# Optimization experiments

Hardware: AMD Instinct MI355X
Metric: run time of the kernel (lower is better)

The kernel has to match this reference:

```python
import jax, jax.numpy as jnp
import numpy as np

B, N, T, C, H = 4, 1024, 12, 256, 8
DK = C // H
SCALE = 1.0 / np.sqrt(DK)


def setup_inputs() -> dict:
    key = jax.random.key(0)
    ks = jax.random.split(key, 16)
    names = ["flow_q", "flow_k", "flow_v", "speed_q", "speed_k", "speed_v"]
    inp = {n: jax.random.normal(ks[i], (B, N, T, C), dtype=jnp.float32) for i, n in enumerate(names)}
    w_scale = 1.0 / np.sqrt(C)  # ~kaiming-uniform-ish magnitude for Linear(C, C)
    wnames = ["w_fq", "w_fk", "w_fv", "w_sq", "w_sk", "w_sv", "w_out"]
    for j, n in enumerate(wnames):
        inp[n] = jax.random.normal(ks[6 + j], (C, C), dtype=jnp.float32) * w_scale
    inp["b_out"] = jnp.zeros((C,), dtype=jnp.float32)
    xav = np.sqrt(2.0 / (T + 1))  # xavier_normal for (T,1) params
    inp["kj"] = jax.random.normal(ks[13], (T, 1), dtype=jnp.float32) * xav
    inp["vf_fs"] = jax.random.normal(ks[14], (T, 1), dtype=jnp.float32) * xav
    return inp


def _heads(x, w):
    # x: [B,N,T,C], w: [C,C] (torch Linear: y = x @ w.T) -> [B,H,N,T,DK]
    y = jnp.einsum('bntc,oc->bnto', x, w)
    return y.reshape(B, N, T, H, DK).transpose(0, 3, 1, 2, 4)


def reference(flow_q, flow_k, flow_v, speed_q, speed_k, speed_v,
              w_fq, w_fk, w_fv, w_sq, w_sk, w_sv, w_out, b_out, kj, vf_fs):
    Qf = _heads(flow_q, w_fq)
    Kf = _heads(flow_k, w_fk)
    Vf = _heads(flow_v, w_fv)
    Qs = _heads(speed_q, w_sq)
    Ks = _heads(speed_k, w_sk)
    Vs = _heads(speed_v, w_sv)

    # FlowSpeed physics transform: Kj * (v - v^2 / (Vf + 1e-5)); (T,1) broadcasts over (T, DK)
    qf_from_speed = kj * (Qs - jnp.square(Qs) / (vf_fs + 1e-5))

    def att(a, b):  # scores over temporal axis: [B,H,N,T,T] -> softmax
        return jax.nn.softmax(jnp.einsum('bhntd,bhnsd->bhnts', a, b) * SCALE, axis=-1)

    def ctx(z, v):
        return jnp.einsum('bhnts,bhnsd->bhntd', z, v)

    z_ff = att(Qf, Kf)
    z_fs = att(Kf, qf_from_speed)
    z_sf = att(Ks, Qf)
    z_ss = att(Qs, Ks)

    def out_proj(c):  # [B,H,N,T,DK] -> [B,N,T,C] -> fc_out (shared weights)
        c = c.transpose(0, 2, 3, 1, 4).reshape(B, N, T, C)
        return jnp.einsum('bntc,oc->bnto', c, w_out) + b_out

    return (out_proj(ctx(z_ff, Vf)),
            out_proj(ctx(z_fs, Vf)),
            out_proj(ctx(z_sf, Vs)),
            out_proj(ctx(z_ss, Vs)))
```

## Files before the change

kernel.cpp:

```cpp
#include <hip/hip_runtime.h>

#define Bn 4
#define Nn 1024
#define Tn 12
#define Cn 256
#define Hn 8
#define DKn 32
#define Mrows 49152
#define NEl 12582912LL
#define SCALE_ 0.17677669529663687f

typedef __attribute__((ext_vector_type(4))) float f32x4;
typedef __attribute__((ext_vector_type(8))) short s16x8;
typedef __attribute__((ext_vector_type(4))) short s16x4;

__device__ __forceinline__ ushort f2bfu(float x) {
    unsigned u = __builtin_bit_cast(unsigned, x);
    u += 0x7fffu + ((u >> 16) & 1u);
    return (ushort)(u >> 16);
}
__device__ __forceinline__ float bfu2f(ushort h) {
    return __builtin_bit_cast(float, ((unsigned)h) << 16);
}

struct WPtrs { const float* src[7]; };

__global__ __launch_bounds__(256)
void wconv_k(WPtrs w, ushort* __restrict__ Wh, ushort* __restrict__ Wl) {
    int idx = blockIdx.x * 256 + threadIdx.x;
    int which = idx >> 16, pos = idx & 65535;
    float x = w.src[which][pos];
    ushort h = f2bfu(x);
    Wh[idx] = h;
    Wl[idx] = f2bfu(x - bfu2f(h));
}

struct GPtrs {
    const void*   A[4];
    const ushort* Wh[4];
    const ushort* Wl[4];
    void*         Y[4];
};

template<bool SPLIT, bool IN_BF16, bool OUT_BF16, bool BIAS>
__global__ __launch_bounds__(256)
void gemm_k(GPtrs p, const float* __restrict__ bias) {
    const int bt   = blockIdx.y;
    const int bm   = blockIdx.x * 64;
    const int tid  = threadIdx.x;
    const int lane = tid & 63;
    const int wave = tid >> 6;

    __shared__ short As[64 * 40];
    __shared__ short Bs[256 * 40];
    __shared__ short Al[SPLIT ? 64 * 40 : 8];
    __shared__ short Bl[SPLIT ? 256 * 40 : 8];

    f32x4 acc[4][4];
#pragma unroll
    for (int i = 0; i < 4; i++)
#pragma unroll
        for (int j = 0; j < 4; j++)
            acc[i][j] = (f32x4){0.f, 0.f, 0.f, 0.f};

    const int r  = tid >> 2;
    const int cq = (tid & 3) * 8;

    for (int k0 = 0; k0 < 256; k0 += 32) {
        if constexpr (IN_BF16) {
            const ushort* A = (const ushort*)p.A[bt];
            s16x8 v = *(const s16x8*)(A + (size_t)(bm + r) * 256 + k0 + cq);
            *(s16x8*)&As[r * 40 + cq] = v;
        } else {
            const float* A = (const float*)p.A[bt];
            const float* g = A + (size_t)(bm + r) * 256 + k0 + cq;
            f32x4 v0 = *(const f32x4*)g;
            f32x4 v1 = *(const f32x4*)(g + 4);
            s16x8 hi, lo;
#pragma unroll
            for (int j = 0; j < 8; j++) {
                float x = (j < 4) ? v0[j] : v1[j - 4];
                ushort hb = f2bfu(x);
                hi[j] = (short)hb;
                if constexpr (SPLIT) lo[j] = (short)f2bfu(x - bfu2f(hb));
            }
            *(s16x8*)&As[r * 40 + cq] = hi;
            if constexpr (SPLIT) *(s16x8*)&Al[r * 40 + cq] = lo;
        }
#pragma unroll
        for (int pw = 0; pw < 4; pw++) {
            int orow = pw * 64 + r;
            *(s16x8*)&Bs[orow * 40 + cq] =
                *(const s16x8*)(p.Wh[bt] + (size_t)orow * 256 + k0 + cq);
            if constexpr (SPLIT)
                *(s16x8*)&Bl[orow * 40 + cq] =
                    *(const s16x8*)(p.Wl[bt] + (size_t)orow * 256 + k0 + cq);
        }
        __syncthreads();
        s16x8 a[4], al[4];
#pragma unroll
        for (int mi = 0; mi < 4; mi++) {
            int off = (mi * 16 + (lane & 15)) * 40 + (lane >> 4) * 8;
            a[mi] = *(const s16x8*)&As[off];
            if constexpr (SPLIT) al[mi] = *(const s16x8*)&Al[off];
        }
#pragma unroll
        for (int ni = 0; ni < 4; ni++) {
            int off = (wave * 64 + ni * 16 + (lane & 15)) * 40 + (lane >> 4) * 8;
            s16x8 b = *(const s16x8*)&Bs[off];
            s16x8 bl;
            if constexpr (SPLIT) bl = *(const s16x8*)&Bl[off];
#pragma unroll
            for (int mi = 0; mi < 4; mi++) {
                acc[mi][ni] = __builtin_amdgcn_mfma_f32_16x16x32_bf16(a[mi], b, acc[mi][ni], 0, 0, 0);
                if constexpr (SPLIT) {
                    acc[mi][ni] = __builtin_amdgcn_mfma_f32_16x16x32_bf16(al[mi], b,  acc[mi][ni], 0, 0, 0);
                    acc[mi][ni] = __builtin_amdgcn_mfma_f32_16x16x32_bf16(a[mi],  bl, acc[mi][ni], 0, 0, 0);
                }
            }
        }
        __syncthreads();
    }
#pragma unroll
    for (int mi = 0; mi < 4; mi++) {
#pragma unroll
        for (int ni = 0; ni < 4; ni++) {
            int col  = wave * 64 + ni * 16 + (lane & 15);
            int row0 = bm + mi * 16 + (lane >> 4) * 4;
            float bv = BIAS ? bias[col] : 0.f;
#pragma unroll
            for (int rg = 0; rg < 4; rg++) {
                float v = acc[mi][ni][rg] + bv;
                size_t idx = (size_t)(row0 + rg) * 256 + col;
                if constexpr (OUT_BF16) ((ushort*)p.Y[bt])[idx] = f2bfu(v);
                else                    ((float*)p.Y[bt])[idx]  = v;
            }
        }
    }
}


#define VSTR 268

__device__ __forceinline__ s16x8 zero8() { s16x8 z = {0,0,0,0,0,0,0,0}; return z; }

__device__ __forceinline__ void split8(f32x4 a, f32x4 b, s16x8& hi, s16x8& lo) {
#pragma unroll
    for (int j = 0; j < 8; j++) {
        float x = (j < 4) ? a[j] : b[j - 4];
        ushort h = f2bfu(x);
        hi[j] = (short)h;
        lo[j] = (short)f2bfu(x - bfu2f(h));
    }
}

__device__ __forceinline__ void softmax_swapped(f32x4 acc, int g, s16x8& ph, s16x8& pl) {
    float x0 = acc[0] * SCALE_, x1 = acc[1] * SCALE_;
    float x2 = acc[2] * SCALE_, x3 = acc[3] * SCALE_;
    float m = fmaxf(fmaxf(x0, x1), fmaxf(x2, x3));
    m = fmaxf(m, __shfl_xor(m, 16));
    m = fmaxf(m, __shfl_xor(m, 32));
    float e0 = expf(x0 - m), e1 = expf(x1 - m), e2 = expf(x2 - m), e3 = expf(x3 - m);
    if (g == 3) { e0 = 0.f; e1 = 0.f; e2 = 0.f; e3 = 0.f; }
    float s = e0 + e1 + e2 + e3;
    s += __shfl_xor(s, 16);
    s += __shfl_xor(s, 32);
    float inv = 1.f / s;
    float p0 = e0 * inv, p1 = e1 * inv, p2 = e2 * inv, p3 = e3 * inv;
    float q0 = __shfl_down(p0, 16), q1 = __shfl_down(p1, 16);
    float q2 = __shfl_down(p2, 16), q3 = __shfl_down(p3, 16);
    float w[8];
    if (g == 0) { w[0]=p0; w[1]=p1; w[2]=p2; w[3]=p3; w[4]=q0; w[5]=q1; w[6]=q2; w[7]=q3; }
    else if (g == 1) { w[0]=q0; w[1]=q1; w[2]=q2; w[3]=q3; w[4]=0.f; w[5]=0.f; w[6]=0.f; w[7]=0.f; }
    else { w[0]=0.f; w[1]=0.f; w[2]=0.f; w[3]=0.f; w[4]=0.f; w[5]=0.f; w[6]=0.f; w[7]=0.f; }
#pragma unroll
    for (int j = 0; j < 8; j++) {
        ushort h = f2bfu(w[j]);
        ph[j] = (short)h;
        pl[j] = (short)f2bfu(w[j] - bfu2f(h));
    }
}

__device__ __forceinline__ s16x8 load_vfrag(const ushort* sV, int col, int g) {
    s16x8 v = zero8();
    if (g < 2) {
#pragma unroll
        for (int j = 0; j < 8; j++) {
            int s = 8 * g + j;
            if (s < 12) v[j] = (short)sV[s * VSTR + col];
        }
    }
    return v;
}

__device__ __forceinline__ void ctx_store(s16x8 ph, s16x8 pl, s16x8 vb0, s16x8 vb1,
                                          ushort* __restrict__ dst, size_t abase,
                                          int g, int r16) {
    f32x4 zf = {0.f, 0.f, 0.f, 0.f};
    f32x4 o0 = __builtin_amdgcn_mfma_f32_16x16x32_bf16(ph, vb0, zf, 0, 0, 0);
    o0 = __builtin_amdgcn_mfma_f32_16x16x32_bf16(pl, vb0, o0, 0, 0, 0);
    f32x4 o1 = __builtin_amdgcn_mfma_f32_16x16x32_bf16(ph, vb1, zf, 0, 0, 0);
    o1 = __builtin_amdgcn_mfma_f32_16x16x32_bf16(pl, vb1, o1, 0, 0, 0);
    if (g < 3) {
#pragma unroll
        for (int rg = 0; rg < 4; rg++) {
            size_t row = (size_t)(4 * g + rg) * Cn;
            dst[abase + row + r16]      = f2bfu(o0[rg]);
            dst[abase + row + 16 + r16] = f2bfu(o1[rg]);
        }
    }
}

__global__ __launch_bounds__(512)
void attn_k(const ushort* __restrict__ Qf, const float* __restrict__ Kf,
            const ushort* __restrict__ Vf, const float* __restrict__ Qs,
            const ushort* __restrict__ Ks, const ushort* __restrict__ Vs,
            const float* __restrict__ kj, const float* __restrict__ vf_fs,
            ushort* __restrict__ c0, ushort* __restrict__ c1,
            ushort* __restrict__ c2, ushort* __restrict__ c3)
{
    const int bn   = blockIdx.x;
    const int tid  = threadIdx.x;
    const int wave = tid >> 6;
    const int lane = tid & 63;
    const int g    = lane >> 4;
    const int r16  = lane & 15;

    __shared__ ushort sVf[12 * VSTR];
    __shared__ ushort sVs[12 * VSTR];

    if (tid < 384) {
        int t = tid >> 5;
        int c = (tid & 31) * 8;
        size_t gb = (size_t)bn * (Tn * Cn) + (size_t)t * Cn + c;
        s16x8 vf8 = *(const s16x8*)(Vf + gb);
        s16x8 vs8 = *(const s16x8*)(Vs + gb);
        s16x4 a0 = {vf8[0], vf8[1], vf8[2], vf8[3]};
        s16x4 a1 = {vf8[4], vf8[5], vf8[6], vf8[7]};
        s16x4 b0 = {vs8[0], vs8[1], vs8[2], vs8[3]};
        s16x4 b1 = {vs8[4], vs8[5], vs8[6], vs8[7]};
        *(s16x4*)&sVf[t * VSTR + c]     = a0;
        *(s16x4*)&sVf[t * VSTR + c + 4] = a1;
        *(s16x4*)&sVs[t * VSTR + c]     = b0;
        *(s16x4*)&sVs[t * VSTR + c + 4] = b1;
    }

    const int  t    = r16;
    const bool tv   = t < 12;
    const int  d0   = g * 8;
    const size_t abase = (size_t)bn * (Tn * Cn) + (size_t)wave * DKn;
    const size_t rb    = abase + (size_t)t * Cn + d0;

    f32x4 z4 = {0.f, 0.f, 0.f, 0.f};
    s16x8 fQf = tv ? *(const s16x8*)(Qf + rb) : zero8();
    s16x8 fKs = tv ? *(const s16x8*)(Ks + rb) : zero8();

    f32x4 kfa = tv ? *(const f32x4*)(Kf + rb)     : z4;
    f32x4 kfb = tv ? *(const f32x4*)(Kf + rb + 4) : z4;
    f32x4 qsa = tv ? *(const f32x4*)(Qs + rb)     : z4;
    f32x4 qsb = tv ? *(const f32x4*)(Qs + rb + 4) : z4;

    s16x8 fKfh, fKfl, fQsh, fQsl;
    split8(kfa, kfb, fKfh, fKfl);
    split8(qsa, qsb, fQsh, fQsl);

    float kjt  = tv ? kj[t]    : 0.f;
    float vft  = tv ? vf_fs[t] : 0.f;
    float invv = 1.f / (vft + 1e-5f);
    f32x4 qfa, qfb;
#pragma unroll
    for (int j = 0; j < 4; j++) {
        float qa = qsa[j], qb = qsb[j];
        qfa[j] = kjt * (qa - qa * qa * invv);
        qfb[j] = kjt * (qb - qb * qb * invv);
    }
    s16x8 fqfh, fqfl;
    split8(qfa, qfb, fqfh, fqfl);

    f32x4 zf = {0.f, 0.f, 0.f, 0.f};
    f32x4 aff = __builtin_amdgcn_mfma_f32_16x16x32_bf16(fKfh, fQf, zf, 0, 0, 0);
    aff = __builtin_amdgcn_mfma_f32_16x16x32_bf16(fKfl, fQf, aff, 0, 0, 0);
    f32x4 afs = __builtin_amdgcn_mfma_f32_16x16x32_bf16(fqfh, fKfh, zf, 0, 0, 0);
    afs = __builtin_amdgcn_mfma_f32_16x16x32_bf16(fqfl, fKfh, afs, 0, 0, 0);
    afs = __builtin_amdgcn_mfma_f32_16x16x32_bf16(fqfh, fKfl, afs, 0, 0, 0);
    afs = __builtin_amdgcn_mfma_f32_16x16x32_bf16(fqfl, fKfl, afs, 0, 0, 0);
    f32x4 asf = __builtin_amdgcn_mfma_f32_16x16x32_bf16(fQf, fKs, zf, 0, 0, 0);
    f32x4 ass = __builtin_amdgcn_mfma_f32_16x16x32_bf16(fKs, fQsh, zf, 0, 0, 0);
    ass = __builtin_amdgcn_mfma_f32_16x16x32_bf16(fKs, fQsl, ass, 0, 0, 0);

    __syncthreads();
    s16x8 vbf0 = load_vfrag(sVf, wave * 32 + r16,      g);
    s16x8 vbf1 = load_vfrag(sVf, wave * 32 + 16 + r16, g);
    s16x8 vbs0 = load_vfrag(sVs, wave * 32 + r16,      g);
    s16x8 vbs1 = load_vfrag(sVs, wave * 32 + 16 + r16, g);

    s16x8 ph, pl;
    softmax_swapped(aff, g, ph, pl);
    ctx_store(ph, pl, vbf0, vbf1, c0, abase, g, r16);
    softmax_swapped(afs, g, ph, pl);
    ctx_store(ph, pl, vbf0, vbf1, c1, abase, g, r16);
    softmax_swapped(asf, g, ph, pl);
    ctx_store(ph, pl, vbs0, vbs1, c2, abase, g, r16);
    softmax_swapped(ass, g, ph, pl);
    ctx_store(ph, pl, vbs0, vbs1, c3, abase, g, r16);
}

extern "C" void kernel_launch(void* const* d_in, const int* in_sizes, int n_in,
                              void* d_out, int out_size, void* d_ws, size_t ws_size,
                              hipStream_t stream) {
    (void)in_sizes; (void)n_in; (void)out_size; (void)ws_size;

    const float* flow_q  = (const float*)d_in[0];
    const float* flow_k  = (const float*)d_in[1];
    const float* flow_v  = (const float*)d_in[2];
    const float* speed_q = (const float*)d_in[3];
    const float* speed_k = (const float*)d_in[4];
    const float* speed_v = (const float*)d_in[5];
    const float* w_fq  = (const float*)d_in[6];
    const float* w_fk  = (const float*)d_in[7];
    const float* w_fv  = (const float*)d_in[8];
    const float* w_sq  = (const float*)d_in[9];
    const float* w_sk  = (const float*)d_in[10];
    const float* w_sv  = (const float*)d_in[11];
    const float* w_out = (const float*)d_in[12];
    const float* b_out = (const float*)d_in[13];
    const float* kj    = (const float*)d_in[14];
    const float* vf    = (const float*)d_in[15];

    char* ws = (char*)d_ws;
    size_t off = 0;
    auto alloc = [&](size_t bytes) -> void* {
        void* p = ws + off;
        off += (bytes + 255) & ~(size_t)255;
        return p;
    };
    ushort* Wh = (ushort*)alloc(7 * 65536 * 2);
    ushort* Wl = (ushort*)alloc(7 * 65536 * 2);
    ushort* Qf = (ushort*)alloc(NEl * 2);
    float*  Kf = (float*) alloc(NEl * 4);
    ushort* Vf = (ushort*)alloc(NEl * 2);
    float*  Qs = (float*) alloc(NEl * 4);
    ushort* Ks = (ushort*)alloc(NEl * 2);
    ushort* Vs = (ushort*)alloc(NEl * 2);
    ushort* c0 = (ushort*)alloc(NEl * 2);
    ushort* c1 = (ushort*)alloc(NEl * 2);
    ushort* c2 = (ushort*)alloc(NEl * 2);
    ushort* c3 = (ushort*)alloc(NEl * 2);

    float* out = (float*)d_out;

    WPtrs wp;
    wp.src[0] = w_fq; wp.src[1] = w_fk; wp.src[2] = w_fv; wp.src[3] = w_sq;
    wp.src[4] = w_sk; wp.src[5] = w_sv; wp.src[6] = w_out;
    wconv_k<<<dim3(7 * 65536 / 256), 256, 0, stream>>>(wp, Wh, Wl);

    GPtrs p1;
    p1.A[0] = flow_q;  p1.Wh[0] = Wh + 0 * 65536; p1.Wl[0] = Wl + 0 * 65536; p1.Y[0] = Qf;
    p1.A[1] = flow_v;  p1.Wh[1] = Wh + 2 * 65536; p1.Wl[1] = Wl + 2 * 65536; p1.Y[1] = Vf;
    p1.A[2] = speed_k; p1.Wh[2] = Wh + 4 * 65536; p1.Wl[2] = Wl + 4 * 65536; p1.Y[2] = Ks;
    p1.A[3] = speed_v; p1.Wh[3] = Wh + 5 * 65536; p1.Wl[3] = Wl + 5 * 65536; p1.Y[3] = Vs;
    gemm_k<false, false, true, false><<<dim3(Mrows / 64, 4), 256, 0, stream>>>(p1, nullptr);

    GPtrs p2;
    p2.A[0] = flow_k;  p2.Wh[0] = Wh + 1 * 65536; p2.Wl[0] = Wl + 1 * 65536; p2.Y[0] = Kf;
    p2.A[1] = speed_q; p2.Wh[1] = Wh + 3 * 65536; p2.Wl[1] = Wl + 3 * 65536; p2.Y[1] = Qs;
    p2.A[2] = flow_k;  p2.Wh[2] = Wh + 1 * 65536; p2.Wl[2] = Wl + 1 * 65536; p2.Y[2] = Kf;
    p2.A[3] = flow_k;  p2.Wh[3] = Wh + 1 * 65536; p2.Wl[3] = Wl + 1 * 65536; p2.Y[3] = Kf;
    gemm_k<true, false, false, false><<<dim3(Mrows / 64, 2), 256, 0, stream>>>(p2, nullptr);

    attn_k<<<dim3(Bn * Nn), 512, 0, stream>>>(Qf, Kf, Vf, Qs, Ks, Vs, kj, vf, c0, c1, c2, c3);

    GPtrs p3;
    p3.A[0] = c0; p3.Wh[0] = Wh + 6 * 65536; p3.Wl[0] = Wl + 6 * 65536; p3.Y[0] = out;
    p3.A[1] = c1; p3.Wh[1] = Wh + 6 * 65536; p3.Wl[1] = Wl + 6 * 65536; p3.Y[1] = out + NEl;
    p3.A[2] = c2; p3.Wh[2] = Wh + 6 * 65536; p3.Wl[2] = Wl + 6 * 65536; p3.Y[2] = out + 2 * NEl;
    p3.A[3] = c3; p3.Wh[3] = Wh + 6 * 65536; p3.Wl[3] = Wl + 6 * 65536; p3.Y[3] = out + 3 * NEl;
    gemm_k<false, true, false, true><<<dim3(Mrows / 64, 4), 256, 0, stream>>>(p3, b_out);
}
```

Baseline: 624.0 us.

## Double-buffer GEMM tiles with direct global-to-LDS loads and XOR swizzle

Restructures the projection GEMMs to use 128-row tiles with 512-thread blocks (8 waves in a 2x4 layout) and double-buffered LDS. Weight and bf16 activation tiles are loaded with global_load_lds straight into shared memory, using an XOR swizzle in place of padding. The aim is to overlap the next K-slice load with the current MFMA work, halve the weight reloads per output row, and avoid bank conflicts. In exchange LDS use per block goes up, especially for the split variant, which can limit occupancy.

```diff
diff --git a/kernel.cpp b/kernel.cpp
--- a/kernel.cpp
+++ b/kernel.cpp
@@ -23,6 +23,12 @@
     return __builtin_bit_cast(float, ((unsigned)h) << 16);
 }
 
+__device__ __forceinline__ void gld_lds16(const void* g, void* l) {
+    __builtin_amdgcn_global_load_lds(
+        (const __attribute__((address_space(1))) unsigned*)g,
+        (__attribute__((address_space(3))) unsigned*)l, 16, 0, 0);
+}
+
 struct WPtrs { const float* src[7]; };
 
 __global__ __launch_bounds__(256)
@@ -43,18 +49,23 @@
 };
 
 template<bool SPLIT, bool IN_BF16, bool OUT_BF16, bool BIAS>
-__global__ __launch_bounds__(256)
-void gemm_k(GPtrs p, const float* __restrict__ bias) {
+__device__ __forceinline__ void gemm_body(GPtrs p, const float* __restrict__ bias) {
     const int bt   = blockIdx.y;
-    const int bm   = blockIdx.x * 64;
+    const int bm   = blockIdx.x * 128;
     const int tid  = threadIdx.x;
     const int lane = tid & 63;
     const int wave = tid >> 6;
-
-    __shared__ short As[64 * 40];
-    __shared__ short Bs[256 * 40];
-    __shared__ short Al[SPLIT ? 64 * 40 : 8];
-    __shared__ short Bl[SPLIT ? 256 * 40 : 8];
+    const int wm   = wave >> 2;
+    const int wn   = wave & 3;
+    const int r16  = lane & 15;
+    const int cbf  = (lane >> 4) * 16;
+
+    constexpr int ASZ = 128 * 32;
+    constexpr int BSZ = 256 * 32;
+    __shared__ ushort Ah[2][ASZ];
+    __shared__ ushort Bh[2][BSZ];
+    __shared__ ushort Al[SPLIT ? 2 : 1][SPLIT ? ASZ : 8];
+    __shared__ ushort Bl[SPLIT ? 2 : 1][SPLIT ? BSZ : 8];
 
     f32x4 acc[4][4];
 #pragma unroll
@@ -63,17 +74,31 @@
         for (int j = 0; j < 4; j++)
             acc[i][j] = (f32x4){0.f, 0.f, 0.f, 0.f};
 
-    const int r  = tid >> 2;
-    const int cq = (tid & 3) * 8;
-
-    for (int k0 = 0; k0 < 256; k0 += 32) {
+    auto stage = [&](int buf, int k0) {
+#pragma unroll
+        for (int c = 0; c < 2; ++c) {
+            int ob = c * 8192 + wave * 1024 + lane * 16;
+            int r  = ob >> 6;
+            int cg = ((ob >> 4) & 3) ^ ((r >> 1) & 3);
+            size_t goff = (size_t)r * 256 + k0 + cg * 8;
+            void* ldst = (char*)&Bh[buf][0] + c * 8192 + wave * 1024;
+            gld_lds16(p.Wh[bt] + goff, ldst);
+            if constexpr (SPLIT) {
+                void* ldstl = (char*)&Bl[buf][0] + c * 8192 + wave * 1024;
+                gld_lds16(p.Wl[bt] + goff, ldstl);
+            }
+        }
         if constexpr (IN_BF16) {
-            const ushort* A = (const ushort*)p.A[bt];
-            s16x8 v = *(const s16x8*)(A + (size_t)(bm + r) * 256 + k0 + cq);
-            *(s16x8*)&As[r * 40 + cq] = v;
+            int ob = wave * 1024 + lane * 16;
+            int r  = ob >> 6;
+            int cg = ((ob >> 4) & 3) ^ ((r >> 1) & 3);
+            const ushort* g = (const ushort*)p.A[bt] + (size_t)(bm + r) * 256 + k0 + cg * 8;
+            void* ldst = (char*)&Ah[buf][0] + wave * 1024;
+            gld_lds16(g, ldst);
         } else {
-            const float* A = (const float*)p.A[bt];
-            const float* g = A + (size_t)(bm + r) * 256 + k0 + cq;
+            int r  = tid >> 2;
+            int cg = (tid & 3) ^ ((r >> 1) & 3);
+            const float* g = (const float*)p.A[bt] + (size_t)(bm + r) * 256 + k0 + cg * 8;
             f32x4 v0 = *(const f32x4*)g;
             f32x4 v1 = *(const f32x4*)(g + 4);
             s16x8 hi, lo;
@@ -84,32 +109,27 @@
                 hi[j] = (short)hb;
                 if constexpr (SPLIT) lo[j] = (short)f2bfu(x - bfu2f(hb));
             }
-            *(s16x8*)&As[r * 40 + cq] = hi;
-            if constexpr (SPLIT) *(s16x8*)&Al[r * 40 + cq] = lo;
-        }
-#pragma unroll
-        for (int pw = 0; pw < 4; pw++) {
-            int orow = pw * 64 + r;
-            *(s16x8*)&Bs[orow * 40 + cq] =
-                *(const s16x8*)(p.Wh[bt] + (size_t)orow * 256 + k0 + cq);
-            if constexpr (SPLIT)
-                *(s16x8*)&Bl[orow * 40 + cq] =
-                    *(const s16x8*)(p.Wl[bt] + (size_t)orow * 256 + k0 + cq);
-        }
-        __syncthreads();
+            *(s16x8*)((char*)&Ah[buf][0] + tid * 16) = hi;
+            if constexpr (SPLIT) *(s16x8*)((char*)&Al[buf][0] + tid * 16) = lo;
+        }
+    };
+
+    auto compute = [&](int buf) {
         s16x8 a[4], al[4];
 #pragma unroll
         for (int mi = 0; mi < 4; mi++) {
-            int off = (mi * 16 + (lane & 15)) * 40 + (lane >> 4) * 8;
-            a[mi] = *(const s16x8*)&As[off];
-            if constexpr (SPLIT) al[mi] = *(const s16x8*)&Al[off];
+            int R   = wm * 64 + mi * 16 + r16;
+            int off = (R * 64 + cbf) ^ (((R >> 1) & 3) << 4);
+            a[mi] = *(const s16x8*)((const char*)&Ah[buf][0] + off);
+            if constexpr (SPLIT) al[mi] = *(const s16x8*)((const char*)&Al[buf][0] + off);
         }
 #pragma unroll
         for (int ni = 0; ni < 4; ni++) {
-            int off = (wave * 64 + ni * 16 + (lane & 15)) * 40 + (lane >> 4) * 8;
-            s16x8 b = *(const s16x8*)&Bs[off];
+            int R   = wn * 64 + ni * 16 + r16;
+            int off = (R * 64 + cbf) ^ (((R >> 1) & 3) << 4);
+            s16x8 b = *(const s16x8*)((const char*)&Bh[buf][0] + off);
             s16x8 bl;
-            if constexpr (SPLIT) bl = *(const s16x8*)&Bl[off];
+            if constexpr (SPLIT) bl = *(const s16x8*)((const char*)&Bl[buf][0] + off);
 #pragma unroll
             for (int mi = 0; mi < 4; mi++) {
                 acc[mi][ni] = __builtin_amdgcn_mfma_f32_16x16x32_bf16(a[mi], b, acc[mi][ni], 0, 0, 0);
@@ -119,14 +139,23 @@
                 }
             }
         }
+    };
+
+    stage(0, 0);
+    __syncthreads();
+#pragma unroll
+    for (int ks = 0; ks < 8; ++ks) {
+        if (ks < 7) stage((ks + 1) & 1, (ks + 1) * 32);
+        compute(ks & 1);
         __syncthreads();
     }
+
 #pragma unroll
     for (int mi = 0; mi < 4; mi++) {
 #pragma unroll
         for (int ni = 0; ni < 4; ni++) {
-            int col  = wave * 64 + ni * 16 + (lane & 15);
-            int row0 = bm + mi * 16 + (lane >> 4) * 4;
+            int col  = wn * 64 + ni * 16 + r16;
+            int row0 = bm + wm * 64 + mi * 16 + (lane >> 4) * 4;
             float bv = BIAS ? bias[col] : 0.f;
 #pragma unroll
             for (int rg = 0; rg < 4; rg++) {
@@ -137,6 +166,17 @@
             }
         }
     }
+}
+
+__global__ __launch_bounds__(512, 4)
+void gemm_proj_k(GPtrs p) { gemm_body<false, false, true, false>(p, nullptr); }
+
+__global__ __launch_bounds__(512, 2)
+void gemm_split_k(GPtrs p) { gemm_body<true, false, false, false>(p, nullptr); }
+
+__global__ __launch_bounds__(512, 4)
+void gemm_out_k(GPtrs p, const float* __restrict__ bias) {
+    gemm_body<false, true, false, true>(p, bias);
 }
 
 
@@ -359,14 +399,14 @@
     p1.A[1] = flow_v;  p1.Wh[1] = Wh + 2 * 65536; p1.Wl[1] = Wl + 2 * 65536; p1.Y[1] = Vf;
     p1.A[2] = speed_k; p1.Wh[2] = Wh + 4 * 65536; p1.Wl[2] = Wl + 4 * 65536; p1.Y[2] = Ks;
     p1.A[3] = speed_v; p1.Wh[3] = Wh + 5 * 65536; p1.Wl[3] = Wl + 5 * 65536; p1.Y[3] = Vs;
-    gemm_k<false, false, true, false><<<dim3(Mrows / 64, 4), 256, 0, stream>>>(p1, nullptr);
+    gemm_proj_k<<<dim3(Mrows / 128, 4), 512, 0, stream>>>(p1);
 
     GPtrs p2;
     p2.A[0] = flow_k;  p2.Wh[0] = Wh + 1 * 65536; p2.Wl[0] = Wl + 1 * 65536; p2.Y[0] = Kf;
     p2.A[1] = speed_q; p2.Wh[1] = Wh + 3 * 65536; p2.Wl[1] = Wl + 3 * 65536; p2.Y[1] = Qs;
     p2.A[2] = flow_k;  p2.Wh[2] = Wh + 1 * 65536; p2.Wl[2] = Wl + 1 * 65536; p2.Y[2] = Kf;
     p2.A[3] = flow_k;  p2.Wh[3] = Wh + 1 * 65536; p2.Wl[3] = Wl + 1 * 65536; p2.Y[3] = Kf;
-    gemm_k<true, false, false, false><<<dim3(Mrows / 64, 2), 256, 0, stream>>>(p2, nullptr);
+    gemm_split_k<<<dim3(Mrows / 128, 2), 512, 0, stream>>>(p2);
 
     attn_k<<<dim3(Bn * Nn), 512, 0, stream>>>(Qf, Kf, Vf, Qs, Ks, Vs, kj, vf, c0, c1, c2, c3);
 
@@ -375,5 +415,5 @@
     p3.A[1] = c1; p3.Wh[1] = Wh + 6 * 65536; p3.Wl[1] = Wl + 6 * 65536; p3.Y[1] = out + NEl;
     p3.A[2] = c2; p3.Wh[2] = Wh + 6 * 65536; p3.Wl[2] = Wl + 6 * 65536; p3.Y[2] = out + 2 * NEl;
     p3.A[3] = c3; p3.Wh[3] = Wh + 6 * 65536; p3.Wl[3] = Wl + 6 * 65536; p3.Y[3] = out + 3 * NEl;
-    gemm_k<false, true, false, true><<<dim3(Mrows / 64, 4), 256, 0, stream>>>(p3, b_out);
-}
+    gemm_out_k<<<dim3(Mrows / 128, 4), 512, 0, stream>>>(p3, b_out);
+}
```

Measured after the change: 601.9 us. 3.5% less time.
